# Kernel optimization log

Hardware: AMD Instinct MI355X
Metric: run time of the kernel (lower is better)

The kernel has to match this reference:

```python
import jax, jax.numpy as jnp
import numpy as np

C = 1024
H = 16
EPS = 1e-5


def setup_inputs() -> dict:
    key = jax.random.key(0)
    ks = jax.random.split(key, 10)
    B, S = 2, 2048
    s = 1.0 / np.sqrt(C)
    return {
        "hidden_states": jax.random.normal(ks[0], (B, C, S), dtype=jnp.float32),
        "attention_mask": jnp.ones((B, S), dtype=jnp.int32),
        "gn_weight": jnp.ones((C,), dtype=jnp.float32),
        "gn_bias": jnp.zeros((C,), dtype=jnp.float32),
        "Wq": jax.random.normal(ks[1], (C, C), dtype=jnp.float32) * s,
        "bq": jnp.zeros((C,), dtype=jnp.float32),
        "Wk": jax.random.normal(ks[2], (C, C), dtype=jnp.float32) * s,
        "bk": jnp.zeros((C,), dtype=jnp.float32),
        "Wv": jax.random.normal(ks[3], (C, C), dtype=jnp.float32) * s,
        "bv": jnp.zeros((C,), dtype=jnp.float32),
        "Wo": jax.random.normal(ks[4], (C, C), dtype=jnp.float32) * s,
        "bo": jnp.zeros((C,), dtype=jnp.float32),
    }


def reference(hidden_states, attention_mask, gn_weight, gn_bias,
              Wq, bq, Wk, bk, Wv, bv, Wo, bo):
    # hidden_states: (B, C, S); attention_mask: (B, S)
    B, Cc, S = hidden_states.shape
    D = Cc // H
    residual = hidden_states

    # GroupNorm with 1 group: normalize over (C, S) per sample
    mean = jnp.mean(hidden_states, axis=(1, 2), keepdims=True)
    var = jnp.var(hidden_states, axis=(1, 2), keepdims=True)
    x = (hidden_states - mean) * jax.lax.rsqrt(var + EPS)
    x = x * gn_weight[None, :, None] + gn_bias[None, :, None]

    x = jnp.transpose(x, (0, 2, 1))  # (B, S, C)
    q = x @ Wq.T + bq
    k = x @ Wk.T + bk
    v = x @ Wv.T + bv

    # (B, H, S, D)
    q = q.reshape(B, S, H, D).transpose(0, 2, 1, 3)
    k = k.reshape(B, S, H, D).transpose(0, 2, 1, 3)
    v = v.reshape(B, S, H, D).transpose(0, 2, 1, 3)

    scale = 1.0 / np.sqrt(np.sqrt(D))
    scores = jnp.einsum('bhqd,bhkd->bhqk', q * scale, k * scale)
    mask = attention_mask[:, None, None, :]  # (B,1,1,S) broadcast over heads/query
    scores = jnp.where(mask == 0, -jnp.inf, scores)
    probs = jax.nn.softmax(scores, axis=-1)

    out = jnp.einsum('bhqk,bhkd->bhqd', probs, v)  # (B,H,S,D)
    out = out.transpose(0, 2, 1, 3).reshape(B, S, Cc)
    out = out @ Wo.T + bo
    out = jnp.transpose(out, (0, 2, 1))  # (B, C, S)
    return out + residual
```

## Files before the change

kernel.cpp:

```cpp
#include <hip/hip_runtime.h>
#include <hip/hip_bf16.h>

#define B_ 2
#define C_ 1024
#define S_ 2048
#define H_ 16
#define KDIM 1024

typedef __attribute__((ext_vector_type(8))) short short8_t;
typedef __attribute__((ext_vector_type(4))) float f32x4;
typedef __attribute__((ext_vector_type(16))) float f32x16;
typedef __attribute__((ext_vector_type(4))) int i32x4;

__device__ __forceinline__ void glds16(const void* g, void* l) {
  __builtin_amdgcn_global_load_lds((const __attribute__((address_space(1))) void*)g,
                                   (__attribute__((address_space(3))) void*)l, 16, 0, 0);
}

__device__ __forceinline__ unsigned short f2bf(float f) {
  __hip_bfloat16 h = __float2bfloat16(f);
  return __builtin_bit_cast(unsigned short, h);
}

__device__ __forceinline__ unsigned pkbf(float lo, float hi) {
  unsigned r;
  asm("v_cvt_pk_bf16_f32 %0, %1, %2" : "=v"(r) : "v"(lo), "v"(hi));
  return r;
}

__device__ __forceinline__ void plswap(unsigned &a, unsigned &b) {
  asm("v_permlane32_swap_b32 %0, %1" : "+v"(a), "+v"(b));
}

__device__ __forceinline__ float max3f(float a, float b, float c) {
  float r;
  asm("v_max3_f32 %0, %1, %2, %3" : "=v"(r) : "v"(a), "v"(b), "v"(c));
  return r;
}

__device__ __forceinline__ float max16v(const f32x16& v) {
  float a = max3f(v[0], v[1], v[2]);
  float b = max3f(v[3], v[4], v[5]);
  float c = max3f(v[6], v[7], v[8]);
  float d = max3f(v[9], v[10], v[11]);
  float e = max3f(v[12], v[13], v[14]);
  float f = max3f(a, b, v[15]);
  float g = max3f(c, d, e);
  return fmaxf(f, g);
}

__global__ __launch_bounds__(256) void cvt_w4(const float* __restrict__ a,
                                              const float* __restrict__ b,
                                              const float* __restrict__ c,
                                              const float* __restrict__ d,
                                              unsigned short* __restrict__ o) {
  int g = blockIdx.x >> 10;
  const float* src = (g == 0) ? a : (g == 1) ? b : (g == 2) ? c : d;
  int i = (blockIdx.x & 1023) * 256 + threadIdx.x;
  float4 v = ((const float4*)src)[i];
  short4 r;
  r.x = (short)f2bf(v.x); r.y = (short)f2bf(v.y);
  r.z = (short)f2bf(v.z); r.w = (short)f2bf(v.w);
  ((short4*)(o))[(size_t)g * 262144 + i] = r;
}

__global__ __launch_bounds__(256) void stats1(const float* __restrict__ x,
                                              float2* __restrict__ part) {
  int bid = blockIdx.x;
  int b = bid >> 8, chunk = bid & 255;
  const float4* p = (const float4*)(x + (size_t)b*(C_*S_) + (size_t)chunk*8192);
  int t = threadIdx.x;
  float s = 0.f, q = 0.f;
#pragma unroll
  for (int i = 0; i < 8; ++i) {
    float4 v = p[t + i*256];
    s += v.x + v.y + v.z + v.w;
    q += v.x*v.x + v.y*v.y + v.z*v.z + v.w*v.w;
  }
#pragma unroll
  for (int d = 1; d < 64; d <<= 1) { s += __shfl_xor(s, d); q += __shfl_xor(q, d); }
  __shared__ float2 wsum[4];
  if ((t & 63) == 0) wsum[t >> 6] = make_float2(s, q);
  __syncthreads();
  if (t == 0) {
    float S = 0.f, Q = 0.f;
    for (int i = 0; i < 4; ++i) { S += wsum[i].x; Q += wsum[i].y; }
    part[bid] = make_float2(S, Q);
  }
}

__global__ __launch_bounds__(256) void normt(const float* __restrict__ x,
                                             const float* __restrict__ gw,
                                             const float* __restrict__ gb,
                                             const float2* __restrict__ part,
                                             unsigned short* __restrict__ xt) {
  __shared__ short lds[64*72];
  __shared__ float2 wsum2[4];
  int bid = blockIdx.x;
  int b = bid >> 9, rem = bid & 511;
  int ct = rem >> 5, st = rem & 31;
  int t = threadIdx.x;

  float2 pv = part[b*256 + t];
  float s = pv.x, q = pv.y;
#pragma unroll
  for (int d = 1; d < 64; d <<= 1) { s += __shfl_xor(s, d); q += __shfl_xor(q, d); }
  if ((t & 63) == 0) wsum2[t >> 6] = make_float2(s, q);
  __syncthreads();
  float S = 0.f, Q = 0.f;
#pragma unroll
  for (int i = 0; i < 4; ++i) { S += wsum2[i].x; Q += wsum2[i].y; }
  const float invN = 1.0f / (float)(C_*S_);
  float mean = S * invN;
  float rstd = rsqrtf(Q * invN - mean*mean + 1e-5f);

  int r = t >> 2, seg = t & 3;
  int c = ct*64 + r;
  float wsc = gw[c] * rstd;
  float bof = gb[c] - mean * wsc;
  const float4* src = (const float4*)(x + (size_t)b*(C_*S_) + (size_t)c*S_ + st*64 + seg*16);
#pragma unroll
  for (int j = 0; j < 4; ++j) {
    float4 v = src[j];
    int sl = seg*16 + j*4;
    lds[(sl+0)*72 + r] = (short)f2bf(v.x*wsc + bof);
    lds[(sl+1)*72 + r] = (short)f2bf(v.y*wsc + bof);
    lds[(sl+2)*72 + r] = (short)f2bf(v.z*wsc + bof);
    lds[(sl+3)*72 + r] = (short)f2bf(v.w*wsc + bof);
  }
  __syncthreads();
  int sl = t >> 2;
  __attribute__((aligned(16))) unsigned short tmp[16];
#pragma unroll
  for (int j = 0; j < 16; ++j) tmp[j] = (unsigned short)lds[sl*72 + seg*16 + j];
  unsigned short* dst = xt + ((size_t)b*S_ + st*64 + sl) * C_ + ct*64 + seg*16;
  *(short8_t*)dst       = *(const short8_t*)tmp;
  *(short8_t*)(dst + 8) = *(const short8_t*)(tmp + 8);
}

__global__ __launch_bounds__(256)
void gemm_qkv(const unsigned short* __restrict__ A,
              const unsigned short* __restrict__ Bm,
              const float* __restrict__ bq,
              const float* __restrict__ bk,
              const float* __restrict__ bv,
              unsigned short* __restrict__ outqk,
              unsigned short* __restrict__ outv) {
  __shared__ __attribute__((aligned(16))) short smem[128*128];
  short* As = smem;
  short* Bs = smem + 8192;
  int bid = blockIdx.x;
  int sbid = (bid & 7) * 96 + (bid >> 3);
  int bm = sbid / 24, bn = sbid % 24;
  int m0 = bm << 7, n0 = bn << 7;
  int t = threadIdx.x, l = t & 63, wid = t >> 6;
  int wr = wid >> 1, wc = wid & 1;

  int rsb = wid*8 + (l >> 3);
  int slot_src = (l & 7) ^ (l >> 3);
  const unsigned short* a_src = A + (size_t)(m0 + rsb) * KDIM + slot_src * 8;
  const unsigned short* b_src = Bm + (size_t)(n0 + rsb) * KDIM + slot_src * 8;
  char* adst = (char*)As + wid*1024;
  char* bdst = (char*)Bs + wid*1024;

  f32x4 acc[4][4] = {};

  for (int kt = 0; kt < KDIM; kt += 64) {
    __syncthreads();
#pragma unroll
    for (int i = 0; i < 4; ++i) {
      glds16(a_src + (size_t)(i*32)*KDIM + kt, adst + i*4096);
      glds16(b_src + (size_t)(i*32)*KDIM + kt, bdst + i*4096);
    }
    __syncthreads();
#pragma unroll
    for (int kk = 0; kk < 2; ++kk) {
      short8_t af[4], bf[4];
#pragma unroll
      for (int mi = 0; mi < 4; ++mi) {
        int row = wr*64 + mi*16 + (l & 15);
        int slot = (kk*4 + (l >> 4)) ^ (row & 7);
        af[mi] = *(const short8_t*)((const char*)As + row*128 + slot*16);
      }
#pragma unroll
      for (int ni = 0; ni < 4; ++ni) {
        int row = wc*64 + ni*16 + (l & 15);
        int slot = (kk*4 + (l >> 4)) ^ (row & 7);
        bf[ni] = *(const short8_t*)((const char*)Bs + row*128 + slot*16);
      }
#pragma unroll
      for (int mi = 0; mi < 4; ++mi)
#pragma unroll
        for (int ni = 0; ni < 4; ++ni)
          acc[mi][ni] = __builtin_amdgcn_mfma_f32_16x16x32_bf16(af[mi], bf[ni], acc[mi][ni], 0, 0, 0);
    }
  }

  if (bn < 16) {
    int gcol0 = n0 + wc*64;
    const float* bp = (gcol0 & 1024) ? bk : bq;
    unsigned short* ob = outqk + ((gcol0 & 1024) ? 4194304u : 0u);
    int hd0 = gcol0 & 1023;
#pragma unroll
    for (int mi = 0; mi < 4; ++mi)
#pragma unroll
      for (int ni = 0; ni < 4; ++ni)
#pragma unroll
        for (int r = 0; r < 4; ++r) {
          int gm = m0 + wr*64 + mi*16 + ((l >> 4) << 2) + r;
          int hd = hd0 + ni*16 + (l & 15);
          float v = acc[mi][ni][r] + bp[hd];
          size_t off = ((size_t)((gm >> 11)*H_ + (hd >> 6)) * S_ + (gm & 2047)) * 64 + (hd & 63);
          ob[off] = f2bf(v);
        }
  } else {
    int hdbase = n0 - 2048;
    __syncthreads();
#pragma unroll
    for (int ni = 0; ni < 4; ++ni) {
      int cl = wc*64 + ni*16 + (l & 15);
      float bvv = bv[hdbase + cl];
#pragma unroll
      for (int mi = 0; mi < 4; ++mi)
#pragma unroll
        for (int r = 0; r < 4; ++r) {
          int rl = wr*64 + mi*16 + ((l >> 4) << 2) + r;
          smem[cl*128 + rl] = (short)f2bf(acc[mi][ni][r] + bvv);
        }
    }
    __syncthreads();
    int b = m0 >> 11, s0 = m0 & 2047;
    int rn = t >> 1, seg = (t & 1) << 6;
    const char* srcp = (const char*)smem + rn*256 + seg*2;
    unsigned short* dstp = outv + ((size_t)(b*1024 + hdbase + rn)) * 2048 + s0 + seg;
#pragma unroll
    for (int j = 0; j < 8; ++j)
      *(i32x4*)(dstp + j*8) = *(const i32x4*)(srcp + j*16);
  }
}

template<int EPI>
__global__ __launch_bounds__(256)
void gemm_nt(const unsigned short* __restrict__ A,
             const unsigned short* __restrict__ Bm,
             const float* __restrict__ bias,
             const float* __restrict__ resid,
             void* __restrict__ outp,
             int nbn) {
  __shared__ __attribute__((aligned(16))) short As[64*64];
  __shared__ __attribute__((aligned(16))) short Bs[128*64];
  int nwg = gridDim.x;
  int bid = blockIdx.x;
  int cpx = nwg >> 3;
  int sbid = (bid & 7) * cpx + (bid >> 3);
  int bm = sbid / nbn, bn = sbid % nbn;
  int m0 = bm << 6, n0 = bn << 7;
  int t = threadIdx.x;
  int l = t & 63, wid = t >> 6;

  int r_st = t >> 3;
  int slot_src = (t & 7) ^ (r_st & 7);
  const unsigned short* a_src = A + (size_t)(m0 + r_st) * KDIM + slot_src * 8;
  const unsigned short* b_src = Bm + (size_t)(n0 + r_st) * KDIM + slot_src * 8;
  char* As_base = (char*)As + wid*1024;
  char* Bs_base = (char*)Bs + wid*1024;

  f32x4 acc[4][2] = {};

  for (int kt = 0; kt < KDIM; kt += 64) {
    __syncthreads();
    glds16(a_src + kt, As_base);
    glds16(a_src + (size_t)32*KDIM + kt, As_base + 4096);
#pragma unroll
    for (int i = 0; i < 4; ++i)
      glds16(b_src + (size_t)(i*32)*KDIM + kt, Bs_base + i*4096);
    __syncthreads();
#pragma unroll
    for (int kk = 0; kk < 2; ++kk) {
      short8_t af[4], bfr[2];
#pragma unroll
      for (int mi = 0; mi < 4; ++mi) {
        int row = mi*16 + (l & 15);
        int slot = (kk*4 + (l >> 4)) ^ (row & 7);
        af[mi] = *(const short8_t*)((const char*)As + row*128 + slot*16);
      }
#pragma unroll
      for (int ni = 0; ni < 2; ++ni) {
        int row = wid*32 + ni*16 + (l & 15);
        int slot = (kk*4 + (l >> 4)) ^ (row & 7);
        bfr[ni] = *(const short8_t*)((const char*)Bs + row*128 + slot*16);
      }
#pragma unroll
      for (int mi = 0; mi < 4; ++mi)
#pragma unroll
        for (int ni = 0; ni < 2; ++ni)
          acc[mi][ni] = __builtin_amdgcn_mfma_f32_16x16x32_bf16(af[mi], bfr[ni], acc[mi][ni], 0, 0, 0);
    }
  }

#pragma unroll
  for (int mi = 0; mi < 4; ++mi) {
#pragma unroll
    for (int ni = 0; ni < 2; ++ni) {
#pragma unroll
      for (int r = 0; r < 4; ++r) {
        int gm = m0 + mi*16 + ((l >> 4) << 2) + r;
        int gn = n0 + wid*32 + ni*16 + (l & 15);
        float v = acc[mi][ni][r];
        v += bias[gm];
        size_t off = (size_t)(gn >> 11) * ((size_t)C_*S_) + (size_t)gm * S_ + (gn & 2047);
        if (EPI == 1) {
          ((unsigned short*)outp)[off] = f2bf(v);
        } else {
          ((float*)outp)[off] = v + resid[off];
        }
      }
    }
  }
}

__global__ __launch_bounds__(512, 4)
void attn_kernel(const unsigned short* __restrict__ Q,
                 const unsigned short* __restrict__ Kt,
                 const unsigned short* __restrict__ Vt,
                 const int* __restrict__ mask,
                 unsigned short* __restrict__ outp) {
  __shared__ __attribute__((aligned(16))) char lds[65536];
  __shared__ __attribute__((aligned(8)))  unsigned char maskb[256];
  __shared__ int tflag[32];

  int bid = blockIdx.x;
  int bid2 = (bid & 7) * 64 + (bid >> 3);
  int bh = bid2 >> 4, qt = bid2 & 15;
  int b = bh >> 4, h = bh & 15;
  int t = threadIdx.x, l = t & 63, wid = t >> 6;
  int quad = wid >> 2, qw = wid & 3;
  int hh = l >> 5;

  if (t < 256) {
    const i32x4* mp = (const i32x4*)(mask + b * S_) + t * 2;
    i32x4 m0 = mp[0], m1 = mp[1];
    unsigned by = (unsigned)(m0[0]!=0) | ((unsigned)(m0[1]!=0)<<1) | ((unsigned)(m0[2]!=0)<<2) | ((unsigned)(m0[3]!=0)<<3)
                | ((unsigned)(m1[0]!=0)<<4) | ((unsigned)(m1[1]!=0)<<5) | ((unsigned)(m1[2]!=0)<<6) | ((unsigned)(m1[3]!=0)<<7);
    maskb[t] = (unsigned char)by;
  }
  __syncthreads();
  if (t < 32) {
    unsigned long long v = ((const unsigned long long*)maskb)[t];
    tflag[t] = (v == 0xFFFFFFFFFFFFFFFFull) ? 1 : 0;
  }

  int q0 = qt*128 + qw*32;
  const unsigned short* qp = Q + ((size_t)bh * S_ + q0 + (l & 31)) * 64 + hh * 8;
  short8_t qf[4];
#pragma unroll
  for (int c = 0; c < 4; ++c) qf[c] = *(const short8_t*)(qp + c*16);

  int kbase = quad << 10;
  int row_st = qw*16 + (l >> 3);
  int slot_st = (l & 7) ^ (l >> 3);
  const unsigned short* kp = Kt + ((size_t)bh * S_ + kbase + row_st) * 64 + slot_st * 8;
  const unsigned short* vp = Vt + ((size_t)bh * 64 + row_st) * S_ + kbase + slot_st * 8;
  char* kdst = lds + quad*16384 + qw*2048;
  char* vdst = kdst + 32768;

  unsigned ko[8];
#pragma unroll
  for (int c = 0; c < 4; ++c) {
    unsigned slot = (unsigned)((c*2 + hh) ^ (l & 7)) * 16u;
    ko[c]   = (unsigned)(quad*16384) + (unsigned)(l & 31)*128u + slot;
    ko[c+4] = ko[c] + 4096u;
  }

  const short8_t vones = {0x3F80, 0x3F80, 0x3F80, 0x3F80, 0x3F80, 0x3F80, 0x3F80, 0x3F80};
  const float SC = 0.18033688011112042f;
  float m_run = 0.f, msc = 0.f;
  f32x16 oc0 = {}, oc1 = {}, lsum = {};

  glds16(kp,                kdst);
  glds16(kp + 8*64,         kdst + 1024);
  glds16(vp,                vdst);
  glds16(vp + (size_t)8*S_, vdst + 1024);
  const unsigned short* kn = kp + 64*64;
  const unsigned short* vn = vp + 64;
  int lt = 0;

#define ATILE(BUF)                                                              \
  do {                                                                          \
    __syncthreads();                                                            \
    glds16(kn,                kdst + ((BUF)^1)*8192);                           \
    glds16(kn + 8*64,         kdst + ((BUF)^1)*8192 + 1024);                    \
    glds16(vn,                vdst + ((BUF)^1)*8192);                           \
    glds16(vn + (size_t)8*S_, vdst + ((BUF)^1)*8192 + 1024);                    \
    kn += 4096; vn += 64;                                                       \
    f32x16 st0 = {}, st1 = {};                                                  \
    __builtin_amdgcn_s_setprio(1);                                              \
    _Pragma("unroll")                                                           \
    for (int c = 0; c < 4; ++c) {                                               \
      short8_t kf0 = *(const short8_t*)(lds + ko[c]   + (BUF)*8192);            \
      short8_t kf1 = *(const short8_t*)(lds + ko[c+4] + (BUF)*8192);            \
      st0 = __builtin_amdgcn_mfma_f32_32x32x16_bf16(kf0, qf[c], st0, 0, 0, 0);  \
      st1 = __builtin_amdgcn_mfma_f32_32x32x16_bf16(kf1, qf[c], st1, 0, 0, 0);  \
    }                                                                           \
    __builtin_amdgcn_s_setprio(0);                                              \
    _Pragma("unroll")                                                           \
    for (int r = 0; r < 16; ++r) {                                              \
      st0[r] = __builtin_amdgcn_exp2f(fmaf(st0[r], SC, -msc));                  \
      st1[r] = __builtin_amdgcn_exp2f(fmaf(st1[r], SC, -msc));                  \
    }                                                                           \
    if (!tflag[(kbase >> 6) + lt]) {                                            \
      _Pragma("unroll")                                                         \
      for (int r = 0; r < 16; ++r) {                                            \
        int kl = kbase + lt*64 + (r & 3) + 8*(r >> 2) + 4*hh;                   \
        if (!((maskb[kl >> 3] >> (kl & 7)) & 1)) st0[r] = 0.f;                  \
        kl += 32;                                                               \
        if (!((maskb[kl >> 3] >> (kl & 7)) & 1)) st1[r] = 0.f;                  \
      }                                                                         \
    }                                                                           \
    float pmax = fmaxf(max16v(st0), max16v(st1));                               \
    short8_t pa[4];                                                             \
    {                                                                           \
      unsigned a0 = pkbf(st0[0],  st0[1]),  b0 = pkbf(st0[4],  st0[5]);         \
      unsigned a1 = pkbf(st0[2],  st0[3]),  b1 = pkbf(st0[6],  st0[7]);         \
      plswap(a0, b0); plswap(a1, b1);                                           \
      i32x4 w0 = {(int)a0, (int)a1, (int)b0, (int)b1};                          \
      pa[0] = __builtin_bit_cast(short8_t, w0);                                 \
      unsigned a2 = pkbf(st0[8],  st0[9]),  b2 = pkbf(st0[12], st0[13]);        \
      unsigned a3 = pkbf(st0[10], st0[11]), b3 = pkbf(st0[14], st0[15]);        \
      plswap(a2, b2); plswap(a3, b3);                                           \
      i32x4 w1 = {(int)a2, (int)a3, (int)b2, (int)b3};                          \
      pa[1] = __builtin_bit_cast(short8_t, w1);                                 \
      unsigned a4 = pkbf(st1[0],  st1[1]),  b4 = pkbf(st1[4],  st1[5]);         \
      unsigned a5 = pkbf(st1[2],  st1[3]),  b5 = pkbf(st1[6],  st1[7]);         \
      plswap(a4, b4); plswap(a5, b5);                                           \
      i32x4 w2 = {(int)a4, (int)a5, (int)b4, (int)b5};                          \
      pa[2] = __builtin_bit_cast(short8_t, w2);                                 \
      unsigned a6 = pkbf(st1[8],  st1[9]),  b6 = pkbf(st1[12], st1[13]);        \
      unsigned a7 = pkbf(st1[10], st1[11]), b7 = pkbf(st1[14], st1[15]);        \
      plswap(a6, b6); plswap(a7, b7);                                           \
      i32x4 w3 = {(int)a6, (int)a7, (int)b6, (int)b7};                          \
      pa[3] = __builtin_bit_cast(short8_t, w3);                                 \
    }                                                                           \
    __builtin_amdgcn_s_setprio(1);                                              \
    _Pragma("unroll")                                                           \
    for (int kc = 0; kc < 4; ++kc) {                                            \
      short8_t vf0 = *(const short8_t*)(lds + ko[kc]   + 32768 + (BUF)*8192);   \
      short8_t vf1 = *(const short8_t*)(lds + ko[kc+4] + 32768 + (BUF)*8192);   \
      oc0 = __builtin_amdgcn_mfma_f32_32x32x16_bf16(vf0, pa[kc], oc0, 0, 0, 0); \
      oc1 = __builtin_amdgcn_mfma_f32_32x32x16_bf16(vf1, pa[kc], oc1, 0, 0, 0); \
      lsum = __builtin_amdgcn_mfma_f32_32x32x16_bf16(vones, pa[kc], lsum, 0, 0, 0); \
    }                                                                           \
    __builtin_amdgcn_s_setprio(0);                                              \
    if (__any(pmax > 148.0f)) {                                                 \
      float pm = fmaxf(pmax, __shfl_xor(pmax, 32));                             \
      float smax = (__log2f(pm) + msc) / SC;                                    \
      float nm = fmaxf(m_run, smax);                                            \
      float fac = __builtin_amdgcn_exp2f((m_run - nm) * SC);                    \
      _Pragma("unroll")                                                         \
      for (int r = 0; r < 16; ++r) { oc0[r] *= fac; oc1[r] *= fac; lsum[r] *= fac; } \
      m_run = nm; msc = nm * SC;                                                \
    }                                                                           \
    ++lt;                                                                       \
  } while (0)

  for (int tp = 0; tp < 8; ++tp) {
    ATILE(0);
    ATILE(1);
  }
#undef ATILE

  __syncthreads();
  if (quad == 1) {
    char* obuf = lds + qw*8192 + l*128;
#pragma unroll
    for (int j = 0; j < 4; ++j) {
      f32x4 u0 = { oc0[4*j], oc0[4*j+1], oc0[4*j+2], oc0[4*j+3] };
      *(f32x4*)(obuf + ((j ^ (l & 7)) * 16)) = u0;
      f32x4 u1 = { oc1[4*j], oc1[4*j+1], oc1[4*j+2], oc1[4*j+3] };
      *(f32x4*)(obuf + (((j+4) ^ (l & 7)) * 16)) = u1;
    }
    *(float2*)(lds + 32768 + (qw*64 + l)*8) = make_float2(lsum[0], m_run);
  }
  __syncthreads();
  if (quad == 0) {
    float2 lm1 = *(const float2*)(lds + 32768 + (qw*64 + l)*8);
    float M  = fmaxf(m_run, lm1.y);
    float a0 = __builtin_amdgcn_exp2f((m_run - M) * SC);
    float a1 = __builtin_amdgcn_exp2f((lm1.y - M) * SC);
    float lc = lsum[0] * a0 + lm1.x * a1;
    float inv = 1.f / lc;
    float s0 = a0 * inv, s1 = a1 * inv;
    const char* obuf = lds + qw*8192 + l*128;
#pragma unroll
    for (int j = 0; j < 4; ++j) {
      f32x4 u0 = *(const f32x4*)(obuf + ((j ^ (l & 7)) * 16));
      oc0[4*j]   = oc0[4*j]  *s0 + u0[0]*s1;
      oc0[4*j+1] = oc0[4*j+1]*s0 + u0[1]*s1;
      oc0[4*j+2] = oc0[4*j+2]*s0 + u0[2]*s1;
      oc0[4*j+3] = oc0[4*j+3]*s0 + u0[3]*s1;
      f32x4 u1 = *(const f32x4*)(obuf + (((j+4) ^ (l & 7)) * 16));
      oc1[4*j]   = oc1[4*j]  *s0 + u1[0]*s1;
      oc1[4*j+1] = oc1[4*j+1]*s0 + u1[1]*s1;
      oc1[4*j+2] = oc1[4*j+2]*s0 + u1[2]*s1;
      oc1[4*j+3] = oc1[4*j+3]*s0 + u1[3]*s1;
    }

    unsigned short* obase = outp + ((size_t)b * S_ + q0 + (l & 31)) * C_ + h*64 + hh*8;
#pragma unroll
    for (int dt = 0; dt < 2; ++dt) {
      const f32x16& oc = dt ? oc1 : oc0;
      unsigned a0w = pkbf(oc[0],  oc[1]),  b0w = pkbf(oc[4],  oc[5]);
      unsigned a1w = pkbf(oc[2],  oc[3]),  b1w = pkbf(oc[6],  oc[7]);
      plswap(a0w, b0w); plswap(a1w, b1w);
      i32x4 w0 = {(int)a0w, (int)a1w, (int)b0w, (int)b1w};
      *(i32x4*)(obase + dt*32) = w0;
      unsigned a2w = pkbf(oc[8],  oc[9]),  b2w = pkbf(oc[12], oc[13]);
      unsigned a3w = pkbf(oc[10], oc[11]), b3w = pkbf(oc[14], oc[15]);
      plswap(a2w, b2w); plswap(a3w, b3w);
      i32x4 w1 = {(int)a2w, (int)a3w, (int)b2w, (int)b3w};
      *(i32x4*)(obase + dt*32 + 16) = w1;
    }
  }
}

extern "C" void kernel_launch(void* const* d_in, const int* in_sizes, int n_in,
                              void* d_out, int out_size, void* d_ws, size_t ws_size,
                              hipStream_t stream) {
  const float* hs = (const float*)d_in[0];
  const int*   msk = (const int*)d_in[1];
  const float* gw = (const float*)d_in[2];
  const float* gb = (const float*)d_in[3];
  const float* Wq = (const float*)d_in[4];
  const float* bq = (const float*)d_in[5];
  const float* Wk = (const float*)d_in[6];
  const float* bk = (const float*)d_in[7];
  const float* Wv = (const float*)d_in[8];
  const float* bv = (const float*)d_in[9];
  const float* Wo = (const float*)d_in[10];
  const float* bo = (const float*)d_in[11];

  char* ws = (char*)d_ws;
  float2* part  = (float2*)(ws + 256);
  unsigned short* wq_b = (unsigned short*)(ws + 8192);
  unsigned short* wk_b = wq_b + 1048576;
  unsigned short* wv_b = wk_b + 1048576;
  unsigned short* wo_b = wv_b + 1048576;
  unsigned short* x_b  = wo_b + 1048576;
  unsigned short* q_b  = x_b  + 4194304;
  unsigned short* k_b  = q_b  + 4194304;
  unsigned short* vt_b = k_b  + 4194304;
  unsigned short* ao_b = vt_b + 4194304;

  cvt_w4<<<4096, 256, 0, stream>>>(Wq, Wk, Wv, Wo, wq_b);

  stats1<<<512, 256, 0, stream>>>(hs, part);
  normt<<<1024, 256, 0, stream>>>(hs, gw, gb, part, x_b);

  gemm_qkv<<<768, 256, 0, stream>>>(x_b, wq_b, bq, bk, bv, q_b, vt_b);

  attn_kernel<<<512, 512, 0, stream>>>(q_b, k_b, vt_b, msk, ao_b);

  gemm_nt<2><<<512, 256, 0, stream>>>(wo_b, ao_b, bo, hs, d_out, 32);
}
```

Baseline: 126.9 us.

## Register-prefetch attention K/V tiles, enlarge output GEMM tile, swizzle V-transpose LDS

The attention kernel no longer uses direct global-to-LDS loads with a barrier at the start of each tile. It prefetches the next K/V tile into registers one tile ahead and writes them to the alternate LDS buffer after compute, followed by a single barrier. The output projection GEMM goes from 64x128 to 128x128 tiles, with 256 workgroups each holding 16 accumulators per wave. The V-transpose epilogue in the QKV GEMM XOR-swizzles its LDS staging to avoid bank conflicts. The trade-offs are more register pressure in attention and fewer, larger workgroups in the output GEMM.

```diff
diff --git a/kernel.cpp b/kernel.cpp
--- a/kernel.cpp
+++ b/kernel.cpp
@@ -220,103 +220,95 @@
     for (int ni = 0; ni < 4; ++ni) {
       int cl = wc*64 + ni*16 + (l & 15);
       float bvv = bv[hdbase + cl];
+      int sw = (cl & 15) << 3;
 #pragma unroll
       for (int mi = 0; mi < 4; ++mi)
 #pragma unroll
         for (int r = 0; r < 4; ++r) {
           int rl = wr*64 + mi*16 + ((l >> 4) << 2) + r;
-          smem[cl*128 + rl] = (short)f2bf(acc[mi][ni][r] + bvv);
+          smem[cl*128 + (rl ^ sw)] = (short)f2bf(acc[mi][ni][r] + bvv);
         }
     }
     __syncthreads();
     int b = m0 >> 11, s0 = m0 & 2047;
     int rn = t >> 1, seg = (t & 1) << 6;
-    const char* srcp = (const char*)smem + rn*256 + seg*2;
+    int sw = (rn & 15) << 3;
     unsigned short* dstp = outv + ((size_t)(b*1024 + hdbase + rn)) * 2048 + s0 + seg;
 #pragma unroll
-    for (int j = 0; j < 8; ++j)
-      *(i32x4*)(dstp + j*8) = *(const i32x4*)(srcp + j*16);
-  }
-}
-
-template<int EPI>
+    for (int j = 0; j < 8; ++j) {
+      const short* srcp = smem + rn*128 + ((seg + j*8) ^ sw);
+      *(i32x4*)(dstp + j*8) = *(const i32x4*)srcp;
+    }
+  }
+}
+
 __global__ __launch_bounds__(256)
-void gemm_nt(const unsigned short* __restrict__ A,
-             const unsigned short* __restrict__ Bm,
-             const float* __restrict__ bias,
-             const float* __restrict__ resid,
-             void* __restrict__ outp,
-             int nbn) {
-  __shared__ __attribute__((aligned(16))) short As[64*64];
+void gemm_o(const unsigned short* __restrict__ A,
+            const unsigned short* __restrict__ Bm,
+            const float* __restrict__ bias,
+            const float* __restrict__ resid,
+            float* __restrict__ outp) {
+  __shared__ __attribute__((aligned(16))) short As[128*64];
   __shared__ __attribute__((aligned(16))) short Bs[128*64];
-  int nwg = gridDim.x;
   int bid = blockIdx.x;
-  int cpx = nwg >> 3;
-  int sbid = (bid & 7) * cpx + (bid >> 3);
-  int bm = sbid / nbn, bn = sbid % nbn;
-  int m0 = bm << 6, n0 = bn << 7;
-  int t = threadIdx.x;
-  int l = t & 63, wid = t >> 6;
-
-  int r_st = t >> 3;
-  int slot_src = (t & 7) ^ (r_st & 7);
-  const unsigned short* a_src = A + (size_t)(m0 + r_st) * KDIM + slot_src * 8;
-  const unsigned short* b_src = Bm + (size_t)(n0 + r_st) * KDIM + slot_src * 8;
-  char* As_base = (char*)As + wid*1024;
-  char* Bs_base = (char*)Bs + wid*1024;
-
-  f32x4 acc[4][2] = {};
+  int sbid = (bid & 7) * 32 + (bid >> 3);
+  int bm = sbid & 7, bn = sbid >> 3;
+  int m0 = bm << 7, n0 = bn << 7;
+  int t = threadIdx.x, l = t & 63, wid = t >> 6;
+  int wr = wid >> 1, wc = wid & 1;
+
+  int rsb = wid*8 + (l >> 3);
+  int slot_src = (l & 7) ^ (l >> 3);
+  const unsigned short* a_src = A + (size_t)(m0 + rsb) * KDIM + slot_src * 8;
+  const unsigned short* b_src = Bm + (size_t)(n0 + rsb) * KDIM + slot_src * 8;
+  char* adst = (char*)As + wid*1024;
+  char* bdst = (char*)Bs + wid*1024;
+
+  f32x4 acc[4][4] = {};
 
   for (int kt = 0; kt < KDIM; kt += 64) {
     __syncthreads();
-    glds16(a_src + kt, As_base);
-    glds16(a_src + (size_t)32*KDIM + kt, As_base + 4096);
-#pragma unroll
-    for (int i = 0; i < 4; ++i)
-      glds16(b_src + (size_t)(i*32)*KDIM + kt, Bs_base + i*4096);
+#pragma unroll
+    for (int i = 0; i < 4; ++i) {
+      glds16(a_src + (size_t)(i*32)*KDIM + kt, adst + i*4096);
+      glds16(b_src + (size_t)(i*32)*KDIM + kt, bdst + i*4096);
+    }
     __syncthreads();
 #pragma unroll
     for (int kk = 0; kk < 2; ++kk) {
-      short8_t af[4], bfr[2];
+      short8_t af[4], bf[4];
 #pragma unroll
       for (int mi = 0; mi < 4; ++mi) {
-        int row = mi*16 + (l & 15);
+        int row = wr*64 + mi*16 + (l & 15);
         int slot = (kk*4 + (l >> 4)) ^ (row & 7);
         af[mi] = *(const short8_t*)((const char*)As + row*128 + slot*16);
       }
 #pragma unroll
-      for (int ni = 0; ni < 2; ++ni) {
-        int row = wid*32 + ni*16 + (l & 15);
+      for (int ni = 0; ni < 4; ++ni) {
+        int row = wc*64 + ni*16 + (l & 15);
         int slot = (kk*4 + (l >> 4)) ^ (row & 7);
-        bfr[ni] = *(const short8_t*)((const char*)Bs + row*128 + slot*16);
+        bf[ni] = *(const short8_t*)((const char*)Bs + row*128 + slot*16);
       }
 #pragma unroll
       for (int mi = 0; mi < 4; ++mi)
 #pragma unroll
-        for (int ni = 0; ni < 2; ++ni)
-          acc[mi][ni] = __builtin_amdgcn_mfma_f32_16x16x32_bf16(af[mi], bfr[ni], acc[mi][ni], 0, 0, 0);
-    }
-  }
-
-#pragma unroll
-  for (int mi = 0; mi < 4; ++mi) {
-#pragma unroll
-    for (int ni = 0; ni < 2; ++ni) {
+        for (int ni = 0; ni < 4; ++ni)
+          acc[mi][ni] = __builtin_amdgcn_mfma_f32_16x16x32_bf16(af[mi], bf[ni], acc[mi][ni], 0, 0, 0);
+    }
+  }
+
+#pragma unroll
+  for (int mi = 0; mi < 4; ++mi)
+#pragma unroll
+    for (int ni = 0; ni < 4; ++ni)
 #pragma unroll
       for (int r = 0; r < 4; ++r) {
-        int gm = m0 + mi*16 + ((l >> 4) << 2) + r;
-        int gn = n0 + wid*32 + ni*16 + (l & 15);
-        float v = acc[mi][ni][r];
-        v += bias[gm];
+        int gm = m0 + wr*64 + mi*16 + ((l >> 4) << 2) + r;
+        int gn = n0 + wc*64 + ni*16 + (l & 15);
+        float v = acc[mi][ni][r] + bias[gm];
         size_t off = (size_t)(gn >> 11) * ((size_t)C_*S_) + (size_t)gm * S_ + (gn & 2047);
-        if (EPI == 1) {
-          ((unsigned short*)outp)[off] = f2bf(v);
-        } else {
-          ((float*)outp)[off] = v + resid[off];
-        }
+        outp[off] = v + resid[off];
       }
-    }
-  }
 }
 
 __global__ __launch_bounds__(512, 4)
@@ -361,7 +353,7 @@
   int slot_st = (l & 7) ^ (l >> 3);
   const unsigned short* kp = Kt + ((size_t)bh * S_ + kbase + row_st) * 64 + slot_st * 8;
   const unsigned short* vp = Vt + ((size_t)bh * 64 + row_st) * S_ + kbase + slot_st * 8;
-  char* kdst = lds + quad*16384 + qw*2048;
+  char* kdst = lds + quad*16384 + qw*2048 + l*16;
   char* vdst = kdst + 32768;
 
   unsigned ko[8];
@@ -377,22 +369,29 @@
   float m_run = 0.f, msc = 0.f;
   f32x16 oc0 = {}, oc1 = {}, lsum = {};
 
-  glds16(kp,                kdst);
-  glds16(kp + 8*64,         kdst + 1024);
-  glds16(vp,                vdst);
-  glds16(vp + (size_t)8*S_, vdst + 1024);
-  const unsigned short* kn = kp + 64*64;
-  const unsigned short* vn = vp + 64;
+  i32x4 kr0, kr1, vr0, vr1;
+  kr0 = *(const i32x4*)(kp);
+  kr1 = *(const i32x4*)(kp + 512);
+  vr0 = *(const i32x4*)(vp);
+  vr1 = *(const i32x4*)(vp + (size_t)8*S_);
+  *(i32x4*)(kdst)        = kr0;
+  *(i32x4*)(kdst + 1024) = kr1;
+  *(i32x4*)(vdst)        = vr0;
+  *(i32x4*)(vdst + 1024) = vr1;
+  kr0 = *(const i32x4*)(kp + 4096);
+  kr1 = *(const i32x4*)(kp + 4096 + 512);
+  vr0 = *(const i32x4*)(vp + 64);
+  vr1 = *(const i32x4*)(vp + 64 + (size_t)8*S_);
+  const unsigned short* kn = kp + 8192;
+  const unsigned short* vn = vp + 128;
+  asm volatile("s_waitcnt lgkmcnt(0)" ::: "memory");
+  __builtin_amdgcn_sched_barrier(0);
+  __builtin_amdgcn_s_barrier();
+  __builtin_amdgcn_sched_barrier(0);
   int lt = 0;
 
 #define ATILE(BUF)                                                              \
   do {                                                                          \
-    __syncthreads();                                                            \
-    glds16(kn,                kdst + ((BUF)^1)*8192);                           \
-    glds16(kn + 8*64,         kdst + ((BUF)^1)*8192 + 1024);                    \
-    glds16(vn,                vdst + ((BUF)^1)*8192);                           \
-    glds16(vn + (size_t)8*S_, vdst + ((BUF)^1)*8192 + 1024);                    \
-    kn += 4096; vn += 64;                                                       \
     f32x16 st0 = {}, st1 = {};                                                  \
     __builtin_amdgcn_s_setprio(1);                                              \
     _Pragma("unroll")                                                           \
@@ -460,6 +459,24 @@
       for (int r = 0; r < 16; ++r) { oc0[r] *= fac; oc1[r] *= fac; lsum[r] *= fac; } \
       m_run = nm; msc = nm * SC;                                                \
     }                                                                           \
+    if (lt < 15) {                                                              \
+                                     \
+      *(i32x4*)(kdst + ((BUF)^1)*8192)        = kr0;                            \
+      *(i32x4*)(kdst + ((BUF)^1)*8192 + 1024) = kr1;                            \
+      *(i32x4*)(vdst + ((BUF)^1)*8192)        = vr0;                            \
+      *(i32x4*)(vdst + ((BUF)^1)*8192 + 1024) = vr1;                            \
+      if (lt < 14) {                                                            \
+        kr0 = *(const i32x4*)(kn);                                              \
+        kr1 = *(const i32x4*)(kn + 512);                                        \
+        vr0 = *(const i32x4*)(vn);                                              \
+        vr1 = *(const i32x4*)(vn + (size_t)8*S_);                               \
+        kn += 4096; vn += 64;                                                   \
+      }                                                                         \
+      asm volatile("s_waitcnt lgkmcnt(0)" ::: "memory");                        \
+      __builtin_amdgcn_sched_barrier(0);                                        \
+      __builtin_amdgcn_s_barrier();                                             \
+      __builtin_amdgcn_sched_barrier(0);                                        \
+    }                                                                           \
     ++lt;                                                                       \
   } while (0)
 
@@ -560,5 +577,5 @@
 
   attn_kernel<<<512, 512, 0, stream>>>(q_b, k_b, vt_b, msk, ao_b);
 
-  gemm_nt<2><<<512, 256, 0, stream>>>(wo_b, ao_b, bo, hs, d_out, 32);
-}
+  gemm_o<<<256, 256, 0, stream>>>(wo_b, ao_b, bo, hs, (float*)d_out);
+}
```

Measured after the change: 142.1 us. +12.0%, slower.
